# Optimization experiments

Hardware: AMD Instinct MI355X
Metric: run time of the kernel (lower is better)

## Reference

```python
import jax, jax.numpy as jnp
import numpy as np

HIDDEN = 1024
QKV = 1024
HEADS = 16
HEAD_DIM = QKV // HEADS
B, S = 4, 4096


def setup_inputs() -> dict:
    key = jax.random.key(0)
    ks = jax.random.split(key, 8)
    s = 1.0 / np.sqrt(HIDDEN)
    return {
        "x": jax.random.normal(ks[0], (B, S, HIDDEN), dtype=jnp.float32),
        "mask": jnp.ones((B, S, 1), dtype=jnp.float32),
        "Wq": jax.random.uniform(ks[1], (HIDDEN, QKV), jnp.float32, -s, s),
        "bq": jax.random.uniform(ks[2], (QKV,), jnp.float32, -s, s),
        "Wk": jax.random.uniform(ks[3], (HIDDEN, QKV), jnp.float32, -s, s),
        "bk": jax.random.uniform(ks[4], (QKV,), jnp.float32, -s, s),
        "Wv": jax.random.uniform(ks[5], (HIDDEN, QKV), jnp.float32, -s, s),
        "bv": jax.random.uniform(ks[6], (QKV,), jnp.float32, -s, s),
    }


def _split_heads(t):
    # [B, S, QKV] -> [B, H, S, D]
    b, s, _ = t.shape
    return t.reshape(b, s, HEADS, HEAD_DIM).transpose(0, 2, 1, 3)


def reference(x, mask, Wq, bq, Wk, bk, Wv, bv):
    q = (x @ Wq + bq) * mask  # [B, S, QKV]
    k = (x @ Wk + bk) * mask
    v = (x @ Wv + bv) * mask
    q, k, v = _split_heads(q), _split_heads(k), _split_heads(v)  # [B,H,S,D]
    # k^T @ v : [B, H, D, D]
    kv = jnp.einsum('bhsd,bhse->bhde', k, v)
    # per-batch norm constant from mask sum
    norm = mask.sum(axis=(-1, -2))  # [B]
    norm = 1.0 / jnp.sqrt(norm * HEAD_DIM)
    kv = kv * norm[:, None, None, None]
    # dropout is identity in eval mode
    out = jnp.einsum('bhsd,bhde->bhse', q, kv)  # [B, H, S, D]
    out = out.transpose(0, 2, 1, 3).reshape(B, S, QKV)
    return out
```

## Files before the change

### kernel.cpp

```cpp
#include <hip/hip_runtime.h>
#include <stdint.h>

#define HIDDEN 1024
#define SEQ 4096
#define BATCH 4
#define HEADS 16
#define HDIM 64
#define M_TOT (BATCH * SEQ)
#define NCH 4
#define NT64 16

typedef __bf16 bf16x8 __attribute__((ext_vector_type(8)));
typedef float f32x4 __attribute__((ext_vector_type(4)));
typedef unsigned short u16x8 __attribute__((ext_vector_type(8)));

static __device__ __forceinline__ unsigned short f2bf(float f) {
  union { float f; uint32_t u; } v; v.f = f;
  uint32_t u = v.u;
  uint32_t r = (u + 0x7fffu + ((u >> 16) & 1u)) >> 16;
  return (unsigned short)r;
}
static __device__ __forceinline__ void load_lds16(const void* g, void* l) {
  __builtin_amdgcn_global_load_lds(
      (__attribute__((address_space(1))) void*)(g),
      (__attribute__((address_space(3))) void*)(l), 16, 0, 0);
}

__global__ __launch_bounds__(256) void prep_k(
    const float* __restrict__ x, unsigned short* __restrict__ xb,
    const float* __restrict__ Wk, const float* __restrict__ Wv,
    unsigned short* __restrict__ Bt,
    const float* __restrict__ bk, const float* __restrict__ bv,
    float* __restrict__ bkv,
    const float* __restrict__ mask, float* __restrict__ norm) {
  const int bid = blockIdx.x;
  const int tid = threadIdx.x;
  __shared__ float ts[64][65];
  if (bid < 8192) {
    int idx = bid * 256 + tid;
    const float4* xv = (const float4*)x;
    float4 a = xv[(size_t)idx * 2];
    float4 b = xv[(size_t)idx * 2 + 1];
    u16x8 o;
    o[0] = f2bf(a.x); o[1] = f2bf(a.y); o[2] = f2bf(a.z); o[3] = f2bf(a.w);
    o[4] = f2bf(b.x); o[5] = f2bf(b.y); o[6] = f2bf(b.z); o[7] = f2bf(b.w);
    *(u16x8*)(xb + (size_t)idx * 8) = o;
  } else if (bid < 8704) {
    int idx = bid - 8192;
    int z = idx >> 8, rem = idx & 255;
    const float* W = z ? Wv : Wk;
    unsigned short* out = Bt + (size_t)z * HIDDEN * HIDDEN;
    int n0 = (rem & 15) * 64, k0 = (rem >> 4) * 64;
    int c = tid & 63, rq = tid >> 6;
    for (int i = 0; i < 16; ++i) {
      int r = i * 4 + rq;
      ts[r][c] = W[(size_t)(k0 + r) * HIDDEN + n0 + c];
    }
    __syncthreads();
    for (int i = 0; i < 16; ++i) {
      int n = i * 4 + rq;
      out[(size_t)(n0 + n) * HIDDEN + k0 + c] = f2bf(ts[c][n]);
    }
  } else if (bid < 8712) {
    int i = (bid - 8704) * 256 + tid;
    bkv[i] = (i < HIDDEN) ? bk[i] : bv[i - HIDDEN];
  } else {
    int b = bid - 8712;
    float s = 0.f;
    for (int i = tid; i < SEQ; i += 256) s += mask[b * SEQ + i];
    for (int off = 32; off; off >>= 1) s += __shfl_down(s, off);
    __shared__ float wsum[4];
    if ((tid & 63) == 0) wsum[tid >> 6] = s;
    __syncthreads();
    if (tid == 0) {
      float t = wsum[0] + wsum[1] + wsum[2] + wsum[3];
      norm[b] = rsqrtf(t * (float)HDIM);
    }
  }
}

template <int OUT_MODE, int PER_BATCH_B>
__global__ __launch_bounds__(512, 2) void gemm256_k(
    const unsigned short* __restrict__ A, const unsigned short* __restrict__ Bt,
    const float* __restrict__ bias, const float* __restrict__ mask,
    void* __restrict__ C, int ldc, int nbn) {
  __shared__ unsigned short smem[65536];

  const int nwg = gridDim.x;
  const int bid = blockIdx.x;
  const int wg = (bid & 7) * (nwg >> 3) + (bid >> 3);
  const int row0 = (wg / nbn) * 256;
  const int col0 = (wg % nbn) * 256;

  const unsigned short* Bbase = Bt;
  const float* biasbase = bias;
  if (PER_BATCH_B) {
    int b = row0 >> 12;
    Bbase = Bt + (size_t)b * HIDDEN * HIDDEN;
    biasbase = bias + b * HIDDEN;
  }

  const int tid = threadIdx.x;
  const int wave = tid >> 6;
  const int lane = tid & 63;
  const int wm = wave >> 2;
  const int wn = wave & 3;
  const int lr = lane & 15;
  const int hi = lane >> 4;

  const int srow = tid >> 3;
  const int scol = ((tid & 7) ^ (srow & 7)) * 8;
  const unsigned short* sA = A + (size_t)(row0 + srow) * HIDDEN + scol;
  const unsigned short* sB = Bbase + (size_t)(col0 + srow) * HIDDEN + scol;
  const int ldst = tid * 8;

#define STAGE(half, tt, isB) { \
    int dst_ = ((tt)&1) * 32768 + (isB) * 16384 + (half) * 8192 + ldst; \
    const unsigned short* src_ = ((isB) ? sB : sA) + (size_t)(half) * 128 * HIDDEN + (tt) * 64; \
    load_lds16(src_, &smem[dst_]); \
    load_lds16(src_ + (size_t)64 * HIDDEN, &smem[dst_ + 4096]); }

  const int chunk0 = (hi ^ (lr & 7)) * 8;
  const int chunk1 = ((4 + hi) ^ (lr & 7)) * 8;
  const int arow = (wm * 128 + lr) * 64;
  const int brow = 16384 + (wn * 64 + lr) * 64;

  f32x4 acc[8][4];
#pragma unroll
  for (int i = 0; i < 8; ++i)
#pragma unroll
    for (int j = 0; j < 4; ++j) acc[i][j] = (f32x4){0.f, 0.f, 0.f, 0.f};

  STAGE(0, 0, 0) STAGE(1, 0, 0) STAGE(0, 0, 1) STAGE(1, 0, 1)
  STAGE(0, 1, 1) STAGE(1, 1, 1)
  asm volatile("s_waitcnt vmcnt(4)" ::: "memory");
  __builtin_amdgcn_s_barrier();

  bf16x8 af[4][2], b0f[2][2], b1f[2][2];
  for (int t = 0; t < NT64; ++t) {
    const int bb = (t & 1) * 32768;
#pragma unroll
    for (int rf = 0; rf < 4; ++rf) {
      af[rf][0] = *(const bf16x8*)&smem[bb + arow + rf * 1024 + chunk0];
      af[rf][1] = *(const bf16x8*)&smem[bb + arow + rf * 1024 + chunk1];
    }
#pragma unroll
    for (int cf = 0; cf < 2; ++cf) {
      b0f[cf][0] = *(const bf16x8*)&smem[bb + brow + cf * 1024 + chunk0];
      b0f[cf][1] = *(const bf16x8*)&smem[bb + brow + cf * 1024 + chunk1];
    }
    if (t + 1 < NT64) STAGE(0, t + 1, 0)
    __builtin_amdgcn_s_setprio(1);
#pragma unroll
    for (int rf = 0; rf < 4; ++rf)
#pragma unroll
      for (int cf = 0; cf < 2; ++cf)
#pragma unroll
        for (int kh = 0; kh < 2; ++kh)
          acc[rf][cf] = __builtin_amdgcn_mfma_f32_16x16x32_bf16(af[rf][kh], b0f[cf][kh], acc[rf][cf], 0, 0, 0);
    __builtin_amdgcn_s_setprio(0);
    asm volatile("" ::: "memory");
    __builtin_amdgcn_s_barrier();
#pragma unroll
    for (int cf = 0; cf < 2; ++cf) {
      b1f[cf][0] = *(const bf16x8*)&smem[bb + brow + 2048 + cf * 1024 + chunk0];
      b1f[cf][1] = *(const bf16x8*)&smem[bb + brow + 2048 + cf * 1024 + chunk1];
    }
    if (t + 1 < NT64) STAGE(1, t + 1, 0)
    __builtin_amdgcn_s_setprio(1);
#pragma unroll
    for (int rf = 0; rf < 4; ++rf)
#pragma unroll
      for (int cf = 0; cf < 2; ++cf)
#pragma unroll
        for (int kh = 0; kh < 2; ++kh)
          acc[rf][2 + cf] = __builtin_amdgcn_mfma_f32_16x16x32_bf16(af[rf][kh], b1f[cf][kh], acc[rf][2 + cf], 0, 0, 0);
    __builtin_amdgcn_s_setprio(0);
    asm volatile("" ::: "memory");
    __builtin_amdgcn_s_barrier();
#pragma unroll
    for (int rf = 0; rf < 4; ++rf) {
      af[rf][0] = *(const bf16x8*)&smem[bb + arow + 4096 + rf * 1024 + chunk0];
      af[rf][1] = *(const bf16x8*)&smem[bb + arow + 4096 + rf * 1024 + chunk1];
    }
    __builtin_amdgcn_s_setprio(1);
#pragma unroll
    for (int rf = 0; rf < 4; ++rf)
#pragma unroll
      for (int cf = 0; cf < 2; ++cf)
#pragma unroll
        for (int kh = 0; kh < 2; ++kh)
          acc[4 + rf][cf] = __builtin_amdgcn_mfma_f32_16x16x32_bf16(af[rf][kh], b0f[cf][kh], acc[4 + rf][cf], 0, 0, 0);
    __builtin_amdgcn_s_setprio(0);
    asm volatile("" ::: "memory");
    __builtin_amdgcn_s_barrier();
    if (t + 2 < NT64) { STAGE(0, t + 2, 1) STAGE(1, t + 2, 1) }
    __builtin_amdgcn_s_setprio(1);
#pragma unroll
    for (int rf = 0; rf < 4; ++rf)
#pragma unroll
      for (int cf = 0; cf < 2; ++cf)
#pragma unroll
        for (int kh = 0; kh < 2; ++kh)
          acc[4 + rf][2 + cf] = __builtin_amdgcn_mfma_f32_16x16x32_bf16(af[rf][kh], b1f[cf][kh], acc[4 + rf][2 + cf], 0, 0, 0);
    __builtin_amdgcn_s_setprio(0);
    if (t < NT64 - 3) asm volatile("s_waitcnt vmcnt(4)" ::: "memory");
    else              asm volatile("s_waitcnt vmcnt(0)" ::: "memory");
    __builtin_amdgcn_s_barrier();
  }

  float bcol[4];
#pragma unroll
  for (int an = 0; an < 4; ++an)
    bcol[an] = biasbase[col0 + wn * 64 + (an >> 1) * 32 + (an & 1) * 16 + lr];

  if (OUT_MODE == 2) {
    const int b = row0 >> 12;
    const int s0 = (row0 & 4095) + wm * 128;
    unsigned short* wt = &smem[wave * 4096];
    unsigned short* KVt = (unsigned short*)C;
#pragma unroll
    for (int half = 0; half < 2; ++half) {
#pragma unroll
      for (int am4 = 0; am4 < 4; ++am4) {
#pragma unroll
        for (int j = 0; j < 4; ++j) {
          int r = am4 * 16 + hi * 4 + j;
          float mrow = mask[row0 + wm * 128 + half * 64 + r];
#pragma unroll
          for (int an = 0; an < 4; ++an) {
            int c = (an >> 1) * 32 + (an & 1) * 16 + lr;
            wt[c * 64 + (r ^ ((c & 7) << 3))] =
                f2bf((acc[half * 4 + am4][an][j] + bcol[an]) * mrow);
          }
        }
      }
      asm volatile("s_waitcnt lgkmcnt(0)" ::: "memory");
#pragma unroll
      for (int i = 0; i < 8; ++i) {
        int flat = i * 64 + lane;
        int c = flat >> 3, rq = flat & 7;
        uint4 vv = *(const uint4*)&wt[c * 64 + ((rq * 8) ^ ((c & 7) << 3))];
        *(uint4*)&KVt[((size_t)(col0 + wn * 64 + c) * 4 + b) * 4096 + s0 + half * 64 + rq * 8] = vv;
      }
      asm volatile("s_waitcnt lgkmcnt(0)" ::: "memory");
    }
  } else {
    float* wf = (float*)&smem[(size_t)wave * 8192];
    float* Cg = (float*)C;
#pragma unroll
    for (int h = 0; h < 2; ++h) {
#pragma unroll
      for (int am4 = 0; am4 < 4; ++am4) {
        int am = h * 4 + am4;
#pragma unroll
        for (int j = 0; j < 4; ++j) {
          int r = am4 * 16 + hi * 4 + j;
          float mrow = mask[row0 + wm * 128 + h * 64 + r];
#pragma unroll
          for (int an = 0; an < 4; ++an) {
            int c = (an >> 1) * 32 + (an & 1) * 16 + lr;
            wf[r * 64 + c] = (acc[am][an][j] + bcol[an]) * mrow;
          }
        }
      }
      asm volatile("s_waitcnt lgkmcnt(0)" ::: "memory");
#pragma unroll
      for (int i = 0; i < 16; ++i) {
        int e4 = i * 64 + lane;
        int r = e4 >> 4, c4 = e4 & 15;
        *(float4*)&Cg[(size_t)(row0 + wm * 128 + h * 64 + r) * ldc + col0 + wn * 64 + c4 * 4] =
            *(const float4*)&wf[r * 64 + c4 * 4];
      }
      asm volatile("s_waitcnt lgkmcnt(0)" ::: "memory");
    }
  }
#undef STAGE
}

__global__ __launch_bounds__(256) void kvpart2_k(const unsigned short* __restrict__ KVt,
                                                 float* __restrict__ part) {
  const int bh = blockIdx.x, ch = blockIdx.y;
  const int b = bh >> 4, h = bh & 15;
  __shared__ unsigned short tl[32768];
  const int tid = threadIdx.x;
  const int wave = tid >> 6, lane = tid & 63;
  const int lr = lane & 15, hi = lane >> 4;

  const int r0 = tid >> 3;
  const int cc0 = ((tid & 7) ^ (r0 & 7)) * 8;
  const int r1 = 32 + r0;
  const int cc1 = ((tid & 7) ^ (r1 & 7)) * 8;
  const unsigned short* A0 = KVt + ((size_t)(h * 64 + r0) * 4 + b) * 4096 + ch * 1024 + cc0;
  const unsigned short* A1 = KVt + ((size_t)(h * 64 + r1) * 4 + b) * 4096 + ch * 1024 + cc1;
  const unsigned short* B0 = KVt + ((size_t)(1024 + h * 64 + r0) * 4 + b) * 4096 + ch * 1024 + cc0;
  const unsigned short* B1 = KVt + ((size_t)(1024 + h * 64 + r1) * 4 + b) * 4096 + ch * 1024 + cc1;

#define KSTAGE(tt) { int bb2 = ((tt) & 3) * 8192; \
    load_lds16(A0 + (tt) * 64, &tl[bb2 + tid * 8]); \
    load_lds16(A1 + (tt) * 64, &tl[bb2 + 2048 + tid * 8]); \
    load_lds16(B0 + (tt) * 64, &tl[bb2 + 4096 + tid * 8]); \
    load_lds16(B1 + (tt) * 64, &tl[bb2 + 6144 + tid * 8]); }

  const int ra = wave * 16 + lr;
  const int aoff = ra * 64;
  const int ach0 = (hi ^ (ra & 7)) * 8, ach1 = ((4 + hi) ^ (ra & 7)) * 8;

  f32x4 acc4[4];
#pragma unroll
  for (int nt = 0; nt < 4; ++nt) acc4[nt] = (f32x4){0.f, 0.f, 0.f, 0.f};

  KSTAGE(0) KSTAGE(1)
  asm volatile("s_waitcnt vmcnt(4)" ::: "memory");
  __builtin_amdgcn_s_barrier();
  for (int t = 0; t < 16; ++t) {
    const int bb = (t & 3) * 8192;
    if (t + 2 < 16) KSTAGE(t + 2)
    bf16x8 a0 = *(const bf16x8*)&tl[bb + aoff + ach0];
    bf16x8 a1 = *(const bf16x8*)&tl[bb + aoff + ach1];
    bf16x8 bf0[4], bf1[4];
#pragma unroll
    for (int nt = 0; nt < 4; ++nt) {
      int rb = nt * 16 + lr;
      bf0[nt] = *(const bf16x8*)&tl[bb + 4096 + rb * 64 + ((hi ^ (rb & 7)) * 8)];
      bf1[nt] = *(const bf16x8*)&tl[bb + 4096 + rb * 64 + (((4 + hi) ^ (rb & 7)) * 8)];
    }
#pragma unroll
    for (int nt = 0; nt < 4; ++nt) {
      acc4[nt] = __builtin_amdgcn_mfma_f32_16x16x32_bf16(a0, bf0[nt], acc4[nt], 0, 0, 0);
      acc4[nt] = __builtin_amdgcn_mfma_f32_16x16x32_bf16(a1, bf1[nt], acc4[nt], 0, 0, 0);
    }
    if (t < 14) asm volatile("s_waitcnt vmcnt(4)" ::: "memory");
    else        asm volatile("s_waitcnt vmcnt(0)" ::: "memory");
    __builtin_amdgcn_s_barrier();
  }
  float* dst = part + ((size_t)ch * 64 + bh) * 4096;
#pragma unroll
  for (int nt = 0; nt < 4; ++nt)
#pragma unroll
    for (int j = 0; j < 4; ++j)
      dst[(wave * 16 + hi * 4 + j) * 64 + nt * 16 + lr] = acc4[nt][j];
#undef KSTAGE
}

__global__ void kvreduce_k(const float* __restrict__ part, const float* __restrict__ norm,
                           float* __restrict__ kv) {
  int idx = blockIdx.x * 256 + threadIdx.x;
  int b = idx >> 16;
  float s = 0.f;
#pragma unroll
  for (int ch = 0; ch < NCH; ++ch) s += part[(size_t)ch * 262144 + idx];
  kv[idx] = s * norm[b];
}

__global__ void bias2_k(const float* __restrict__ bq, const float* __restrict__ kv,
                        float* __restrict__ bias2) {
  int idx = blockIdx.x * 256 + threadIdx.x;
  int b = idx >> 10, n = idx & 1023, h = n >> 6, e = n & 63;
  const float* kvp = kv + ((size_t)(b * 16 + h)) * 4096 + e;
  float s = 0.f;
#pragma unroll
  for (int d = 0; d < 64; ++d) s += bq[h * 64 + d] * kvp[d * 64];
  bias2[idx] = s;
}

__global__ __launch_bounds__(128) void wprime_k(const float* __restrict__ Wq,
                                                const float* __restrict__ kv,
                                                unsigned short* __restrict__ Wpt) {
  int bh = blockIdx.y, b = bh >> 4, h = bh & 15;
  int c0 = blockIdx.x * 128;
  __shared__ float wqs[128][65];
  __shared__ float kvs[64][64];
  int tid = threadIdx.x;
  for (int i = 0; i < 32; ++i) {
    int idx = i * 128 + tid;
    ((float*)kvs)[idx] = kv[(size_t)bh * 4096 + idx];
  }
  int rr = tid >> 6, cc = tid & 63;
  for (int i = 0; i < 64; ++i) {
    int r = i * 2 + rr;
    wqs[r][cc] = Wq[(size_t)(c0 + r) * HIDDEN + h * 64 + cc];
  }
  __syncthreads();
  float acc[64];
#pragma unroll
  for (int e = 0; e < 64; ++e) acc[e] = 0.f;
  for (int d = 0; d < 64; ++d) {
    float w = wqs[tid][d];
#pragma unroll
    for (int e4 = 0; e4 < 64; e4 += 4) {
      f32x4 kvv = *(const f32x4*)&kvs[d][e4];
      acc[e4 + 0] += w * kvv[0];
      acc[e4 + 1] += w * kvv[1];
      acc[e4 + 2] += w * kvv[2];
      acc[e4 + 3] += w * kvv[3];
    }
  }
  unsigned short* dst = Wpt + (size_t)b * HIDDEN * HIDDEN + (size_t)(h * 64) * HIDDEN + (c0 + tid);
#pragma unroll
  for (int e = 0; e < 64; ++e) dst[(size_t)e * HIDDEN] = f2bf(acc[e]);
}

extern "C" void kernel_launch(void* const* d_in, const int* in_sizes, int n_in,
                              void* d_out, int out_size, void* d_ws, size_t ws_size,
                              hipStream_t stream) {
  const float* x = (const float*)d_in[0];
  const float* mask = (const float*)d_in[1];
  const float* Wq = (const float*)d_in[2];
  const float* bq = (const float*)d_in[3];
  const float* Wk = (const float*)d_in[4];
  const float* bk = (const float*)d_in[5];
  const float* Wv = (const float*)d_in[6];
  const float* bv = (const float*)d_in[7];
  float* out = (float*)d_out;

  char* w = (char*)d_ws;
  unsigned short* xb = (unsigned short*)w;  w += (size_t)M_TOT * HIDDEN * 2;
  unsigned short* Bt = (unsigned short*)w;  w += (size_t)2048 * HIDDEN * 2;
  unsigned short* KVt = (unsigned short*)w; w += (size_t)2048 * BATCH * SEQ * 2;
  float* part = (float*)w;                  w += (size_t)NCH * 64 * 4096 * 4;
  float* kv = (float*)w;                    w += (size_t)64 * 4096 * 4;
  unsigned short* Wpt = (unsigned short*)w; w += (size_t)BATCH * HIDDEN * HIDDEN * 2;
  float* bkv = (float*)w;                   w += 2048 * 4;
  float* bias2 = (float*)w;                 w += 4096 * 4;
  float* norm = (float*)w;                  w += 64;

  prep_k<<<dim3(8716), dim3(256), 0, stream>>>(x, xb, Wk, Wv, Bt, bk, bv, bkv, mask, norm);
  gemm256_k<2, 0><<<dim3(512), dim3(512), 0, stream>>>(xb, Bt, bkv, mask, (void*)KVt, 0, 8);
  kvpart2_k<<<dim3(64, NCH), dim3(256), 0, stream>>>(KVt, part);
  kvreduce_k<<<dim3(1024), dim3(256), 0, stream>>>(part, norm, kv);
  bias2_k<<<dim3(16), dim3(256), 0, stream>>>(bq, kv, bias2);
  wprime_k<<<dim3(8, 64), dim3(128), 0, stream>>>(Wq, kv, Wpt);
  gemm256_k<0, 1><<<dim3(256), dim3(512), 0, stream>>>(xb, Wpt, bias2, mask, (void*)out, 1024, 4);
}
```

Baseline: 168.6 us.

## Fuse KV reduction and bias into fewer kernels, remap tiles, use nontemporal stores

Removes the split-K partial/reduce kernels for K^T V and has one block per (batch, head) walk the full sequence, applying the norm in its epilogue. The bias2 computation moves into wprime_k, which now stages its bf16 output in LDS for coalesced 16-byte stores. The GEMM tile-to-XCD mapping is changed to a fixed per-XCD column assignment. The output epilogue drops the LDS staging in favour of direct nontemporal scalar stores, and the KVt stores also become nontemporal. These cut launches and intermediate traffic, but the KV kernel now runs only 64 blocks with a longer serial loop, and the direct scalar stores may coalesce worse.

```diff
diff --git a/kernel.cpp b/kernel.cpp
--- a/kernel.cpp
+++ b/kernel.cpp
@@ -7,12 +7,12 @@
 #define HEADS 16
 #define HDIM 64
 #define M_TOT (BATCH * SEQ)
-#define NCH 4
 #define NT64 16
 
 typedef __bf16 bf16x8 __attribute__((ext_vector_type(8)));
 typedef float f32x4 __attribute__((ext_vector_type(4)));
 typedef unsigned short u16x8 __attribute__((ext_vector_type(8)));
+typedef unsigned int u32x4 __attribute__((ext_vector_type(4)));
 
 static __device__ __forceinline__ unsigned short f2bf(float f) {
   union { float f; uint32_t u; } v; v.f = f;
@@ -86,11 +86,19 @@
     void* __restrict__ C, int ldc, int nbn) {
   __shared__ unsigned short smem[65536];
 
-  const int nwg = gridDim.x;
   const int bid = blockIdx.x;
-  const int wg = (bid & 7) * (nwg >> 3) + (bid >> 3);
-  const int row0 = (wg / nbn) * 256;
-  const int col0 = (wg % nbn) * 256;
+  const int xcd = bid & 7;
+  const int idx = bid >> 3;
+  int rowt, colt;
+  if (nbn == 8) {
+    colt = xcd;
+    rowt = (idx + xcd * 8) & 63;
+  } else {
+    colt = xcd >> 1;
+    rowt = ((xcd & 1) * 32 + idx + (xcd >> 1) * 16) & 63;
+  }
+  const int row0 = rowt * 256;
+  const int col0 = colt * 256;
 
   const unsigned short* Bbase = Bt;
   const float* biasbase = bias;
@@ -240,47 +248,38 @@
       for (int i = 0; i < 8; ++i) {
         int flat = i * 64 + lane;
         int c = flat >> 3, rq = flat & 7;
-        uint4 vv = *(const uint4*)&wt[c * 64 + ((rq * 8) ^ ((c & 7) << 3))];
-        *(uint4*)&KVt[((size_t)(col0 + wn * 64 + c) * 4 + b) * 4096 + s0 + half * 64 + rq * 8] = vv;
+        u32x4 vv = *(const u32x4*)&wt[c * 64 + ((rq * 8) ^ ((c & 7) << 3))];
+        __builtin_nontemporal_store(vv,
+            (u32x4*)&KVt[((size_t)(col0 + wn * 64 + c) * 4 + b) * 4096 + s0 + half * 64 + rq * 8]);
       }
       asm volatile("s_waitcnt lgkmcnt(0)" ::: "memory");
     }
   } else {
-    float* wf = (float*)&smem[(size_t)wave * 8192];
     float* Cg = (float*)C;
 #pragma unroll
-    for (int h = 0; h < 2; ++h) {
-#pragma unroll
-      for (int am4 = 0; am4 < 4; ++am4) {
-        int am = h * 4 + am4;
-#pragma unroll
-        for (int j = 0; j < 4; ++j) {
-          int r = am4 * 16 + hi * 4 + j;
-          float mrow = mask[row0 + wm * 128 + h * 64 + r];
-#pragma unroll
-          for (int an = 0; an < 4; ++an) {
-            int c = (an >> 1) * 32 + (an & 1) * 16 + lr;
-            wf[r * 64 + c] = (acc[am][an][j] + bcol[an]) * mrow;
-          }
+    for (int am = 0; am < 8; ++am) {
+      int rbase = (am >> 2) * 64 + (am & 3) * 16 + hi * 4;
+#pragma unroll
+      for (int j = 0; j < 4; ++j) {
+        int r = rbase + j;
+        float mrow = mask[row0 + wm * 128 + r];
+#pragma unroll
+        for (int an = 0; an < 4; ++an) {
+          int c = (an >> 1) * 32 + (an & 1) * 16 + lr;
+          __builtin_nontemporal_store(
+              (acc[am][an][j] + bcol[an]) * mrow,
+              &Cg[(size_t)(row0 + wm * 128 + r) * ldc + col0 + wn * 64 + c]);
         }
       }
-      asm volatile("s_waitcnt lgkmcnt(0)" ::: "memory");
-#pragma unroll
-      for (int i = 0; i < 16; ++i) {
-        int e4 = i * 64 + lane;
-        int r = e4 >> 4, c4 = e4 & 15;
-        *(float4*)&Cg[(size_t)(row0 + wm * 128 + h * 64 + r) * ldc + col0 + wn * 64 + c4 * 4] =
-            *(const float4*)&wf[r * 64 + c4 * 4];
-      }
-      asm volatile("s_waitcnt lgkmcnt(0)" ::: "memory");
     }
   }
 #undef STAGE
 }
 
-__global__ __launch_bounds__(256) void kvpart2_k(const unsigned short* __restrict__ KVt,
-                                                 float* __restrict__ part) {
-  const int bh = blockIdx.x, ch = blockIdx.y;
+__global__ __launch_bounds__(256) void kvpart3_k(const unsigned short* __restrict__ KVt,
+                                                 const float* __restrict__ norm,
+                                                 float* __restrict__ kv) {
+  const int bh = blockIdx.x;
   const int b = bh >> 4, h = bh & 15;
   __shared__ unsigned short tl[32768];
   const int tid = threadIdx.x;
@@ -291,10 +290,10 @@
   const int cc0 = ((tid & 7) ^ (r0 & 7)) * 8;
   const int r1 = 32 + r0;
   const int cc1 = ((tid & 7) ^ (r1 & 7)) * 8;
-  const unsigned short* A0 = KVt + ((size_t)(h * 64 + r0) * 4 + b) * 4096 + ch * 1024 + cc0;
-  const unsigned short* A1 = KVt + ((size_t)(h * 64 + r1) * 4 + b) * 4096 + ch * 1024 + cc1;
-  const unsigned short* B0 = KVt + ((size_t)(1024 + h * 64 + r0) * 4 + b) * 4096 + ch * 1024 + cc0;
-  const unsigned short* B1 = KVt + ((size_t)(1024 + h * 64 + r1) * 4 + b) * 4096 + ch * 1024 + cc1;
+  const unsigned short* A0 = KVt + ((size_t)(h * 64 + r0) * 4 + b) * 4096 + cc0;
+  const unsigned short* A1 = KVt + ((size_t)(h * 64 + r1) * 4 + b) * 4096 + cc1;
+  const unsigned short* B0 = KVt + ((size_t)(1024 + h * 64 + r0) * 4 + b) * 4096 + cc0;
+  const unsigned short* B1 = KVt + ((size_t)(1024 + h * 64 + r1) * 4 + b) * 4096 + cc1;
 
 #define KSTAGE(tt) { int bb2 = ((tt) & 3) * 8192; \
     load_lds16(A0 + (tt) * 64, &tl[bb2 + tid * 8]); \
@@ -313,9 +312,9 @@
   KSTAGE(0) KSTAGE(1)
   asm volatile("s_waitcnt vmcnt(4)" ::: "memory");
   __builtin_amdgcn_s_barrier();
-  for (int t = 0; t < 16; ++t) {
+  for (int t = 0; t < 64; ++t) {
     const int bb = (t & 3) * 8192;
-    if (t + 2 < 16) KSTAGE(t + 2)
+    if (t + 2 < 64) KSTAGE(t + 2)
     bf16x8 a0 = *(const bf16x8*)&tl[bb + aoff + ach0];
     bf16x8 a1 = *(const bf16x8*)&tl[bb + aoff + ach1];
     bf16x8 bf0[4], bf1[4];
@@ -330,58 +329,45 @@
       acc4[nt] = __builtin_amdgcn_mfma_f32_16x16x32_bf16(a0, bf0[nt], acc4[nt], 0, 0, 0);
       acc4[nt] = __builtin_amdgcn_mfma_f32_16x16x32_bf16(a1, bf1[nt], acc4[nt], 0, 0, 0);
     }
-    if (t < 14) asm volatile("s_waitcnt vmcnt(4)" ::: "memory");
+    if (t < 62) asm volatile("s_waitcnt vmcnt(4)" ::: "memory");
     else        asm volatile("s_waitcnt vmcnt(0)" ::: "memory");
     __builtin_amdgcn_s_barrier();
   }
-  float* dst = part + ((size_t)ch * 64 + bh) * 4096;
+  const float nb = norm[b];
+  float* dst = kv + (size_t)bh * 4096;
 #pragma unroll
   for (int nt = 0; nt < 4; ++nt)
 #pragma unroll
     for (int j = 0; j < 4; ++j)
-      dst[(wave * 16 + hi * 4 + j) * 64 + nt * 16 + lr] = acc4[nt][j];
+      dst[(wave * 16 + hi * 4 + j) * 64 + nt * 16 + lr] = acc4[nt][j] * nb;
 #undef KSTAGE
-}
-
-__global__ void kvreduce_k(const float* __restrict__ part, const float* __restrict__ norm,
-                           float* __restrict__ kv) {
-  int idx = blockIdx.x * 256 + threadIdx.x;
-  int b = idx >> 16;
-  float s = 0.f;
-#pragma unroll
-  for (int ch = 0; ch < NCH; ++ch) s += part[(size_t)ch * 262144 + idx];
-  kv[idx] = s * norm[b];
-}
-
-__global__ void bias2_k(const float* __restrict__ bq, const float* __restrict__ kv,
-                        float* __restrict__ bias2) {
-  int idx = blockIdx.x * 256 + threadIdx.x;
-  int b = idx >> 10, n = idx & 1023, h = n >> 6, e = n & 63;
-  const float* kvp = kv + ((size_t)(b * 16 + h)) * 4096 + e;
-  float s = 0.f;
-#pragma unroll
-  for (int d = 0; d < 64; ++d) s += bq[h * 64 + d] * kvp[d * 64];
-  bias2[idx] = s;
 }
 
 __global__ __launch_bounds__(128) void wprime_k(const float* __restrict__ Wq,
                                                 const float* __restrict__ kv,
-                                                unsigned short* __restrict__ Wpt) {
+                                                const float* __restrict__ bq,
+                                                unsigned short* __restrict__ Wpt,
+                                                float* __restrict__ bias2) {
   int bh = blockIdx.y, b = bh >> 4, h = bh & 15;
   int c0 = blockIdx.x * 128;
   __shared__ float wqs[128][65];
   __shared__ float kvs[64][64];
+  __shared__ unsigned short wout[64][128];
   int tid = threadIdx.x;
-  for (int i = 0; i < 32; ++i) {
-    int idx = i * 128 + tid;
-    ((float*)kvs)[idx] = kv[(size_t)bh * 4096 + idx];
-  }
+  for (int i = 0; i < 32; ++i)
+    ((float*)kvs)[i * 128 + tid] = kv[(size_t)bh * 4096 + i * 128 + tid];
   int rr = tid >> 6, cc = tid & 63;
   for (int i = 0; i < 64; ++i) {
     int r = i * 2 + rr;
     wqs[r][cc] = Wq[(size_t)(c0 + r) * HIDDEN + h * 64 + cc];
   }
   __syncthreads();
+  if (blockIdx.x == 0 && tid < 64) {
+    float s = 0.f;
+#pragma unroll
+    for (int d = 0; d < 64; ++d) s += bq[h * 64 + d] * kvs[d][tid];
+    bias2[b * 1024 + h * 64 + tid] = s;
+  }
   float acc[64];
 #pragma unroll
   for (int e = 0; e < 64; ++e) acc[e] = 0.f;
@@ -396,9 +382,14 @@
       acc[e4 + 3] += w * kvv[3];
     }
   }
-  unsigned short* dst = Wpt + (size_t)b * HIDDEN * HIDDEN + (size_t)(h * 64) * HIDDEN + (c0 + tid);
-#pragma unroll
-  for (int e = 0; e < 64; ++e) dst[(size_t)e * HIDDEN] = f2bf(acc[e]);
+#pragma unroll
+  for (int e = 0; e < 64; ++e) wout[e][tid] = f2bf(acc[e]);
+  __syncthreads();
+  unsigned short* dstb = Wpt + (size_t)b * HIDDEN * HIDDEN + (size_t)(h * 64) * HIDDEN + c0;
+  for (int i = tid; i < 1024; i += 128) {
+    int r = i >> 4, q = i & 15;
+    *(uint4*)&dstb[(size_t)r * HIDDEN + q * 8] = *(const uint4*)&wout[r][q * 8];
+  }
 }
 
 extern "C" void kernel_launch(void* const* d_in, const int* in_sizes, int n_in,
@@ -418,7 +409,6 @@
   unsigned short* xb = (unsigned short*)w;  w += (size_t)M_TOT * HIDDEN * 2;
   unsigned short* Bt = (unsigned short*)w;  w += (size_t)2048 * HIDDEN * 2;
   unsigned short* KVt = (unsigned short*)w; w += (size_t)2048 * BATCH * SEQ * 2;
-  float* part = (float*)w;                  w += (size_t)NCH * 64 * 4096 * 4;
   float* kv = (float*)w;                    w += (size_t)64 * 4096 * 4;
   unsigned short* Wpt = (unsigned short*)w; w += (size_t)BATCH * HIDDEN * HIDDEN * 2;
   float* bkv = (float*)w;                   w += 2048 * 4;
@@ -427,9 +417,7 @@
 
   prep_k<<<dim3(8716), dim3(256), 0, stream>>>(x, xb, Wk, Wv, Bt, bk, bv, bkv, mask, norm);
   gemm256_k<2, 0><<<dim3(512), dim3(512), 0, stream>>>(xb, Bt, bkv, mask, (void*)KVt, 0, 8);
-  kvpart2_k<<<dim3(64, NCH), dim3(256), 0, stream>>>(KVt, part);
-  kvreduce_k<<<dim3(1024), dim3(256), 0, stream>>>(part, norm, kv);
-  bias2_k<<<dim3(16), dim3(256), 0, stream>>>(bq, kv, bias2);
-  wprime_k<<<dim3(8, 64), dim3(128), 0, stream>>>(Wq, kv, Wpt);
+  kvpart3_k<<<dim3(64), dim3(256), 0, stream>>>(KVt, norm, kv);
+  wprime_k<<<dim3(8, 64), dim3(128), 0, stream>>>(Wq, kv, bq, Wpt, bias2);
   gemm256_k<0, 1><<<dim3(256), dim3(512), 0, stream>>>(xb, Wpt, bias2, mask, (void*)out, 1024, 4);
 }
```

Result: slower. 192.6 us (+14.2%).
